# Kernel optimization log

Measured on AMD Instinct MI355X. Metric: run time of the kernel, lower is better.

The kernel has to match this reference:

```python
import jax, jax.numpy as jnp
import numpy as np

QUERY_DIM = 192
KEY_DIM = 64
DIM_OUT = 128
C = QUERY_DIM + KEY_DIM  # 256
N = 10000
E = 320000
M = 5000


def setup_inputs() -> dict:
    key = jax.random.key(0)
    ks = jax.random.split(key, 16)
    s = 1.0 / np.sqrt(C)
    inp = {
        "query": jax.random.normal(ks[0], (N, QUERY_DIM), jnp.float32),
        "key_idx": jax.random.randint(ks[1], (N,), 0, KEY_DIM),
        "edge_index": jax.random.randint(ks[2], (2, E), 0, N),
        "mask_idx": jnp.sort(jax.random.randint(ks[3], (M,), 0, N)),
        "Wq": jax.random.normal(ks[4], (C, C), jnp.float32) * s,
        "bq": jnp.zeros((C,), jnp.float32),
        "Wk": jax.random.normal(ks[5], (C, C), jnp.float32) * s,
        "bk": jnp.zeros((C,), jnp.float32),
        "Wv": jax.random.normal(ks[6], (C, C), jnp.float32) * s,
        "bv": jnp.zeros((C,), jnp.float32),
        "Ws": jax.random.normal(ks[7], (C, C), jnp.float32) * s,
        "bs": jnp.zeros((C,), jnp.float32),
        "Wo": jax.random.normal(ks[8], (KEY_DIM, DIM_OUT), jnp.float32) * (1.0 / np.sqrt(KEY_DIM)),
        "bo": jnp.zeros((DIM_OUT,), jnp.float32),
    }
    return inp


def reference(query, key_idx, edge_index, mask_idx, Wq, bq, Wk, bk, Wv, bv, Ws, bs, Wo, bo):
    # node features: [N, C] = concat(query, one_hot(key))
    x = jnp.concatenate([query, jax.nn.one_hot(key_idx, KEY_DIM, dtype=query.dtype)], axis=1)
    src, dst = edge_index[0], edge_index[1]  # messages flow src -> dst
    # node-level projections (dense GEMMs), then edge gather
    q_n = x @ Wq + bq
    k_n = x @ Wk + bk
    v_n = x @ Wv + bv
    q = q_n[dst]  # [E, C]
    k = k_n[src]
    v = v_n[src]
    score = jnp.sum(q * k, axis=-1) / jnp.sqrt(jnp.asarray(C, x.dtype))  # [E]
    # per-destination softmax over incoming edges
    m = jax.ops.segment_max(score, dst, num_segments=N)  # [N]
    m = jnp.where(jnp.isfinite(m), m, 0.0)
    e = jnp.exp(score - m[dst])
    denom = jax.ops.segment_sum(e, dst, num_segments=N)
    alpha = e / (denom[dst] + 1e-16)
    # scatter-aggregate weighted values + root/skip connection
    agg = jax.ops.segment_sum(alpha[:, None] * v, dst, num_segments=N)  # [N, C]
    out = agg + (x @ Ws + bs)
    h = jax.nn.relu(out[mask_idx])  # [M, C]
    h = h[:, QUERY_DIM:]  # [M, KEY_DIM]
    return h @ Wo + bo  # [M, DIM_OUT]
```

## Files before the change

### kernel.cpp

```cpp
#include <hip/hip_runtime.h>

#define QDIM 192
#define KDIM 64
#define CDIM 256
#define NCOLS 640
#define DOUT 128
#define CAP 128
#define NEG_INF __int_as_float(0xFF800000)

typedef _Float16 hf2 __attribute__((ext_vector_type(2)));
typedef _Float16 half4 __attribute__((ext_vector_type(4)));
typedef _Float16 half8 __attribute__((ext_vector_type(8)));
typedef float floatx4 __attribute__((ext_vector_type(4)));

#if defined(__has_builtin)
#if __has_builtin(__builtin_amdgcn_fdot2)
#define HAVE_FDOT2 1
#endif
#endif

__device__ __forceinline__ hf2 bc_h2(unsigned u) { return __builtin_bit_cast(hf2, u); }

__device__ __forceinline__ float dot2acc(hf2 a, hf2 b, float c) {
#ifdef HAVE_FDOT2
    return __builtin_amdgcn_fdot2(a, b, c, false);
#else
    return c + (float)a[0] * (float)b[0] + (float)a[1] * (float)b[1];
#endif
}

__device__ __forceinline__ void wmap(int j, const float* Wq, const float* Wk,
                                     const float* Wv, const float* Ws,
                                     const float** W, int* wcol) {
    if (j < 256)      { *W = Wq; *wcol = j; }
    else if (j < 512) { *W = Wk; *wcol = j - 256; }
    else if (j < 576) { *W = Wv; *wcol = QDIM + (j - 512); }
    else              { *W = Ws; *wcol = QDIM + (j - 576); }
}

__global__ __launch_bounds__(256) void prep_kernel(
        const float* __restrict__ query,
        const float* Wq, const float* Wk, const float* Wv, const float* Ws,
        _Float16* __restrict__ Qh, _Float16* __restrict__ BhT,
        int* __restrict__ deg, int qchunks, int N) {
    int t = blockIdx.x * blockDim.x + threadIdx.x;
    if (t < qchunks) {
        float4 v = ((const float4*)query)[t];
        half4 h = { (_Float16)v.x, (_Float16)v.y, (_Float16)v.z, (_Float16)v.w };
        ((half4*)Qh)[t] = h;
        return;
    }
    t -= qchunks;
    if (t < NCOLS * QDIM) {
        int n = t / QDIM, k = t % QDIM;
        const float* W; int wc;
        wmap(n, Wq, Wk, Wv, Ws, &W, &wc);
        BhT[t] = (_Float16)W[k * CDIM + wc];
        return;
    }
    t -= NCOLS * QDIM;
    if (t < N) deg[t] = 0;
}

__global__ __launch_bounds__(256) void gemm_scatter(
        const _Float16* __restrict__ Qh, const _Float16* __restrict__ BhT,
        const int* __restrict__ key_idx,
        const float* Wq, const float* bq, const float* Wk, const float* bk,
        const float* Wv, const float* bv, const float* Ws, const float* bs,
        const int* __restrict__ esrc, const int* __restrict__ edst,
        int* __restrict__ deg, int* __restrict__ adj, int E,
        _Float16* __restrict__ Qbuf, _Float16* __restrict__ Kbuf,
        _Float16* __restrict__ Vbuf, float* __restrict__ Sbuf, int N) {
    int tid = threadIdx.x;
    int bm = blockIdx.x * 64;

    {
        int total = gridDim.x * gridDim.y * 256;
        int gid = (blockIdx.y * gridDim.x + blockIdx.x) * 256 + tid;
        for (int e = gid; e < E; e += total) {
            int d = edst[e];
            int slot = atomicAdd(&deg[d], 1);
            if (slot < CAP) adj[d * CAP + slot] = esrc[e];
        }
    }

    int w = tid >> 6, l = tid & 63;
    int lrow = l & 15, quad = l >> 4;

    int gr_a = bm + w * 16 + lrow;
    half8 af[6];
    {
        const _Float16* ap = Qh + (size_t)gr_a * QDIM + quad * 8;
        bool ok = (gr_a < N);
        #pragma unroll
        for (int ks = 0; ks < 6; ks++) {
            half8 z = { (_Float16)0.f, (_Float16)0.f, (_Float16)0.f, (_Float16)0.f,
                        (_Float16)0.f, (_Float16)0.f, (_Float16)0.f, (_Float16)0.f };
            af[ks] = ok ? *(const half8*)(ap + ks * 32) : z;
        }
    }

    int ki[4];
    #pragma unroll
    for (int reg = 0; reg < 4; reg++) {
        int gr = bm + w * 16 + quad * 4 + reg;
        ki[reg] = (gr < N) ? key_idx[gr] : 0;
    }

    #pragma unroll
    for (int t = 0; t < 2; t++) {
        int bn = blockIdx.y * 128 + t * 64;
        const float* Wb; const float* bvec; int wc0;
        if (bn < 256)      { Wb = Wq; bvec = bq; wc0 = bn; }
        else if (bn < 512) { Wb = Wk; bvec = bk; wc0 = bn - 256; }
        else if (bn < 576) { Wb = Wv; bvec = bv; wc0 = QDIM + (bn - 512); }
        else               { Wb = Ws; bvec = bs; wc0 = QDIM + (bn - 576); }

        floatx4 acc[4] = {{0.f,0.f,0.f,0.f},{0.f,0.f,0.f,0.f},{0.f,0.f,0.f,0.f},{0.f,0.f,0.f,0.f}};
        const _Float16* bp = BhT + (size_t)(bn + lrow) * QDIM + quad * 8;
        #pragma unroll
        for (int ks = 0; ks < 6; ks++) {
            #pragma unroll
            for (int nt = 0; nt < 4; nt++) {
                half8 bf = *(const half8*)(bp + (size_t)nt * 16 * QDIM + ks * 32);
                acc[nt] = __builtin_amdgcn_mfma_f32_16x16x32_f16(af[ks], bf, acc[nt], 0, 0, 0);
            }
        }

        #pragma unroll
        for (int nt = 0; nt < 4; nt++) {
            int gc = bn + nt * 16 + lrow;
            int wc = wc0 + nt * 16 + lrow;
            float bias = bvec[wc];
            #pragma unroll
            for (int reg = 0; reg < 4; reg++) {
                int gr = bm + w * 16 + quad * 4 + reg;
                if (gr < N) {
                    float v = acc[nt][reg] + Wb[(size_t)(QDIM + ki[reg]) * CDIM + wc] + bias;
                    if (gc < 256)      Qbuf[(size_t)gr * 256 + gc] = (_Float16)v;
                    else if (gc < 512) Kbuf[(size_t)gr * 256 + (gc - 256)] = (_Float16)v;
                    else if (gc < 576) Vbuf[(size_t)gr * KDIM + (gc - 512)] = (_Float16)v;
                    else               Sbuf[(size_t)gr * KDIM + (gc - 576)] = v;
                }
            }
        }
    }
}

__global__ __launch_bounds__(256) void attend_out(
        const _Float16* __restrict__ Qbuf, const _Float16* __restrict__ Kbuf,
        const _Float16* __restrict__ Vbuf, const float* __restrict__ Sbuf,
        const int* __restrict__ deg, const int* __restrict__ adj,
        const int* __restrict__ mask, const float* __restrict__ Wo,
        const float* __restrict__ bo, float* __restrict__ out, int M) {
    int w = threadIdx.x >> 6, lane = threadIdx.x & 63;
    int r = blockIdx.x * 4 + w;
    if (r >= M) return;
    int node = mask[r];
    if (r > 0 && mask[r - 1] == node) return;
    int l = lane & 15, g = lane >> 4;

    const uint4* qp = (const uint4*)(Qbuf + (size_t)node * 256 + l * 16);
    uint4 qa = qp[0], qb = qp[1];
    hf2 qh[8] = { bc_h2(qa.x), bc_h2(qa.y), bc_h2(qa.z), bc_h2(qa.w),
                  bc_h2(qb.x), bc_h2(qb.y), bc_h2(qb.z), bc_h2(qb.w) };

    int dn = min(deg[node], CAP);
    const int* arow = adj + (size_t)node * CAP;

    float m = NEG_INF, dsum = 0.f;
    float a0 = 0.f, a1 = 0.f, a2 = 0.f, a3 = 0.f;
    for (int i = g; i < dn; i += 4) {
        int s = arow[i];
        const uint4* kp = (const uint4*)(Kbuf + (size_t)s * 256 + l * 16);
        uint4 ka = kp[0], kb = kp[1];
        float d = 0.f;
        d = dot2acc(bc_h2(ka.x), qh[0], d);
        d = dot2acc(bc_h2(ka.y), qh[1], d);
        d = dot2acc(bc_h2(ka.z), qh[2], d);
        d = dot2acc(bc_h2(ka.w), qh[3], d);
        d = dot2acc(bc_h2(kb.x), qh[4], d);
        d = dot2acc(bc_h2(kb.y), qh[5], d);
        d = dot2acc(bc_h2(kb.z), qh[6], d);
        d = dot2acc(bc_h2(kb.w), qh[7], d);
        d += __shfl_xor(d, 1, 64);
        d += __shfl_xor(d, 2, 64);
        d += __shfl_xor(d, 4, 64);
        d += __shfl_xor(d, 8, 64);
        float sc = d * 0.0625f;
        float m_new = fmaxf(m, sc);
        float scale = __expf(m - m_new);
        float p = __expf(sc - m_new);
        dsum = dsum * scale + p;
        uint2 vv = *(const uint2*)(Vbuf + (size_t)s * KDIM + l * 4);
        hf2 v01 = bc_h2(vv.x), v23 = bc_h2(vv.y);
        a0 = a0 * scale + p * (float)v01[0];
        a1 = a1 * scale + p * (float)v01[1];
        a2 = a2 * scale + p * (float)v23[0];
        a3 = a3 * scale + p * (float)v23[1];
        m = m_new;
    }

    float Mx = fmaxf(m, __shfl_xor(m, 16, 64));
    Mx = fmaxf(Mx, __shfl_xor(Mx, 32, 64));
    float wgt = (m == NEG_INF) ? 0.f : __expf(m - Mx);
    float ds = dsum * wgt;
    ds += __shfl_xor(ds, 16, 64);
    ds += __shfl_xor(ds, 32, 64);
    a0 *= wgt; a1 *= wgt; a2 *= wgt; a3 *= wgt;
    a0 += __shfl_xor(a0, 16, 64); a0 += __shfl_xor(a0, 32, 64);
    a1 += __shfl_xor(a1, 16, 64); a1 += __shfl_xor(a1, 32, 64);
    a2 += __shfl_xor(a2, 16, 64); a2 += __shfl_xor(a2, 32, 64);
    a3 += __shfl_xor(a3, 16, 64); a3 += __shfl_xor(a3, 32, 64);
    float inv = 1.f / (ds + 1e-16f);

    float4 s4 = *((const float4*)(Sbuf + (size_t)node * KDIM + l * 4));
    float h0 = fmaxf(a0 * inv + s4.x, 0.f);
    float h1 = fmaxf(a1 * inv + s4.y, 0.f);
    float h2 = fmaxf(a2 * inv + s4.z, 0.f);
    float h3 = fmaxf(a3 * inv + s4.w, 0.f);

    float o0 = bo[lane], o1 = bo[lane + 64];
    #pragma unroll
    for (int c = 0; c < KDIM; c++) {
        float hc = (c & 3) == 0 ? h0 : (c & 3) == 1 ? h1 : (c & 3) == 2 ? h2 : h3;
        float hv = __shfl(hc, c >> 2, 64);
        o0 += hv * Wo[c * DOUT + lane];
        o1 += hv * Wo[c * DOUT + 64 + lane];
    }
    int rr = r;
    do {
        out[(size_t)rr * DOUT + lane] = o0;
        out[(size_t)rr * DOUT + 64 + lane] = o1;
        rr++;
    } while (rr < M && mask[rr] == node);
}

extern "C" void kernel_launch(void* const* d_in, const int* in_sizes, int n_in,
                              void* d_out, int out_size, void* d_ws, size_t ws_size,
                              hipStream_t stream) {
    const float* query    = (const float*)d_in[0];
    const int* key_idx    = (const int*)d_in[1];
    const int* edge_index = (const int*)d_in[2];
    const int* mask_idx   = (const int*)d_in[3];
    const float* Wq = (const float*)d_in[4];
    const float* bq = (const float*)d_in[5];
    const float* Wk = (const float*)d_in[6];
    const float* bk = (const float*)d_in[7];
    const float* Wv = (const float*)d_in[8];
    const float* bv = (const float*)d_in[9];
    const float* Ws = (const float*)d_in[10];
    const float* bs = (const float*)d_in[11];
    const float* Wo = (const float*)d_in[12];
    const float* bo = (const float*)d_in[13];

    int N = in_sizes[0] / QDIM;
    int E = in_sizes[2] / 2;
    int M = in_sizes[3];
    const int* esrc = edge_index;
    const int* edst = edge_index + E;

    char* wsb = (char*)d_ws;
    size_t off = 0;
    auto alloc = [&](size_t nbytes) { char* p = wsb + off; off += (nbytes + 15) & ~15ull; return p; };
    _Float16* Qh   = (_Float16*)alloc((size_t)N * QDIM * 2);
    _Float16* BhT  = (_Float16*)alloc((size_t)NCOLS * QDIM * 2);
    _Float16* Qbuf = (_Float16*)alloc((size_t)N * 256 * 2);
    _Float16* Kbuf = (_Float16*)alloc((size_t)N * 256 * 2);
    _Float16* Vbuf = (_Float16*)alloc((size_t)N * KDIM * 2);
    float* Sbuf    = (float*)alloc((size_t)N * KDIM * 4);
    int*   deg     = (int*)alloc((size_t)N * 4);
    int*   adj     = (int*)alloc((size_t)N * CAP * 4);

    int qchunks = N * QDIM / 4;
    int prep_elems = qchunks + NCOLS * QDIM + N;
    prep_kernel<<<(prep_elems + 255) / 256, 256, 0, stream>>>(
        query, Wq, Wk, Wv, Ws, Qh, BhT, deg, qchunks, N);

    dim3 ggrid((N + 63) / 64, 5);
    gemm_scatter<<<ggrid, 256, 0, stream>>>(Qh, BhT, key_idx, Wq, bq, Wk, bk, Wv, bv,
                                            Ws, bs, esrc, edst, deg, adj, E,
                                            Qbuf, Kbuf, Vbuf, Sbuf, N);

    attend_out<<<(M + 3) / 4, 256, 0, stream>>>(Qbuf, Kbuf, Vbuf, Sbuf, deg, adj,
                                                mask_idx, Wo, bo, (float*)d_out, M);
}
```

Baseline: 157.8 us.

## Split edge scatter into own kernel, skip edges to unmasked nodes, shrink adjacency

The edge-bucketing atomics move out of the GEMM kernel into a separate scatter kernel. The degree array is initialised to a large negative sentinel and reset to zero only for masked destination nodes, so edges whose destination is never read skip the atomic and the adjacency write. Adjacency indices are stored as 16-bit values, halving that traffic, and the GEMM grid now uses one 64-column tile per block for more parallelism. This adds a kernel launch and relies on node ids fitting in 16 bits (N=10000 does).

```diff
diff --git a/kernel.cpp b/kernel.cpp
--- a/kernel.cpp
+++ b/kernel.cpp
@@ -59,30 +59,29 @@
         return;
     }
     t -= NCOLS * QDIM;
-    if (t < N) deg[t] = 0;
-}
-
-__global__ __launch_bounds__(256) void gemm_scatter(
+    if (t < N) deg[t] = (int)0x80000000;
+}
+
+__global__ __launch_bounds__(256) void gemm_nodes(
         const _Float16* __restrict__ Qh, const _Float16* __restrict__ BhT,
         const int* __restrict__ key_idx,
         const float* Wq, const float* bq, const float* Wk, const float* bk,
         const float* Wv, const float* bv, const float* Ws, const float* bs,
-        const int* __restrict__ esrc, const int* __restrict__ edst,
-        int* __restrict__ deg, int* __restrict__ adj, int E,
+        const int* __restrict__ mask, int M, int* __restrict__ deg,
         _Float16* __restrict__ Qbuf, _Float16* __restrict__ Kbuf,
         _Float16* __restrict__ Vbuf, float* __restrict__ Sbuf, int N) {
     int tid = threadIdx.x;
     int bm = blockIdx.x * 64;
-
-    {
-        int total = gridDim.x * gridDim.y * 256;
-        int gid = (blockIdx.y * gridDim.x + blockIdx.x) * 256 + tid;
-        for (int e = gid; e < E; e += total) {
-            int d = edst[e];
-            int slot = atomicAdd(&deg[d], 1);
-            if (slot < CAP) adj[d * CAP + slot] = esrc[e];
-        }
-    }
+    int bn = blockIdx.y * 64;
+
+    int gid = (blockIdx.y * gridDim.x + blockIdx.x) * 256 + tid;
+    if (gid < M) deg[mask[gid]] = 0;
+
+    const float* Wb; const float* bvec; int wc0;
+    if (bn < 256)      { Wb = Wq; bvec = bq; wc0 = bn; }
+    else if (bn < 512) { Wb = Wk; bvec = bk; wc0 = bn - 256; }
+    else if (bn < 576) { Wb = Wv; bvec = bv; wc0 = QDIM + (bn - 512); }
+    else               { Wb = Ws; bvec = bs; wc0 = QDIM + (bn - 576); }
 
     int w = tid >> 6, l = tid & 63;
     int lrow = l & 15, quad = l >> 4;
@@ -100,49 +99,51 @@
         }
     }
 
+    floatx4 acc[4] = {{0.f,0.f,0.f,0.f},{0.f,0.f,0.f,0.f},{0.f,0.f,0.f,0.f},{0.f,0.f,0.f,0.f}};
+    const _Float16* bp = BhT + (size_t)(bn + lrow) * QDIM + quad * 8;
+    #pragma unroll
+    for (int ks = 0; ks < 6; ks++) {
+        #pragma unroll
+        for (int nt = 0; nt < 4; nt++) {
+            half8 bf = *(const half8*)(bp + (size_t)nt * 16 * QDIM + ks * 32);
+            acc[nt] = __builtin_amdgcn_mfma_f32_16x16x32_f16(af[ks], bf, acc[nt], 0, 0, 0);
+        }
+    }
+
     int ki[4];
     #pragma unroll
     for (int reg = 0; reg < 4; reg++) {
         int gr = bm + w * 16 + quad * 4 + reg;
         ki[reg] = (gr < N) ? key_idx[gr] : 0;
     }
-
-    #pragma unroll
-    for (int t = 0; t < 2; t++) {
-        int bn = blockIdx.y * 128 + t * 64;
-        const float* Wb; const float* bvec; int wc0;
-        if (bn < 256)      { Wb = Wq; bvec = bq; wc0 = bn; }
-        else if (bn < 512) { Wb = Wk; bvec = bk; wc0 = bn - 256; }
-        else if (bn < 576) { Wb = Wv; bvec = bv; wc0 = QDIM + (bn - 512); }
-        else               { Wb = Ws; bvec = bs; wc0 = QDIM + (bn - 576); }
-
-        floatx4 acc[4] = {{0.f,0.f,0.f,0.f},{0.f,0.f,0.f,0.f},{0.f,0.f,0.f,0.f},{0.f,0.f,0.f,0.f}};
-        const _Float16* bp = BhT + (size_t)(bn + lrow) * QDIM + quad * 8;
+    #pragma unroll
+    for (int nt = 0; nt < 4; nt++) {
+        int gc = bn + nt * 16 + lrow;
+        int wc = wc0 + nt * 16 + lrow;
+        float bias = bvec[wc];
         #pragma unroll
-        for (int ks = 0; ks < 6; ks++) {
-            #pragma unroll
-            for (int nt = 0; nt < 4; nt++) {
-                half8 bf = *(const half8*)(bp + (size_t)nt * 16 * QDIM + ks * 32);
-                acc[nt] = __builtin_amdgcn_mfma_f32_16x16x32_f16(af[ks], bf, acc[nt], 0, 0, 0);
+        for (int reg = 0; reg < 4; reg++) {
+            int gr = bm + w * 16 + quad * 4 + reg;
+            if (gr < N) {
+                float v = acc[nt][reg] + Wb[(size_t)(QDIM + ki[reg]) * CDIM + wc] + bias;
+                if (gc < 256)      Qbuf[(size_t)gr * 256 + gc] = (_Float16)v;
+                else if (gc < 512) Kbuf[(size_t)gr * 256 + (gc - 256)] = (_Float16)v;
+                else if (gc < 576) Vbuf[(size_t)gr * KDIM + (gc - 512)] = (_Float16)v;
+                else               Sbuf[(size_t)gr * KDIM + (gc - 576)] = v;
             }
         }
-
-        #pragma unroll
-        for (int nt = 0; nt < 4; nt++) {
-            int gc = bn + nt * 16 + lrow;
-            int wc = wc0 + nt * 16 + lrow;
-            float bias = bvec[wc];
-            #pragma unroll
-            for (int reg = 0; reg < 4; reg++) {
-                int gr = bm + w * 16 + quad * 4 + reg;
-                if (gr < N) {
-                    float v = acc[nt][reg] + Wb[(size_t)(QDIM + ki[reg]) * CDIM + wc] + bias;
-                    if (gc < 256)      Qbuf[(size_t)gr * 256 + gc] = (_Float16)v;
-                    else if (gc < 512) Kbuf[(size_t)gr * 256 + (gc - 256)] = (_Float16)v;
-                    else if (gc < 576) Vbuf[(size_t)gr * KDIM + (gc - 512)] = (_Float16)v;
-                    else               Sbuf[(size_t)gr * KDIM + (gc - 576)] = v;
-                }
-            }
+    }
+}
+
+__global__ __launch_bounds__(256) void scatter_kernel(
+        const int* __restrict__ src, const int* __restrict__ dst,
+        int* __restrict__ deg, unsigned short* __restrict__ adj, int E) {
+    int e = blockIdx.x * blockDim.x + threadIdx.x;
+    if (e < E) {
+        int d = dst[e];
+        if (deg[d] > -1000000) {
+            int slot = atomicAdd(&deg[d], 1);
+            if ((unsigned)slot < CAP) adj[(size_t)d * CAP + slot] = (unsigned short)src[e];
         }
     }
 }
@@ -150,7 +151,7 @@
 __global__ __launch_bounds__(256) void attend_out(
         const _Float16* __restrict__ Qbuf, const _Float16* __restrict__ Kbuf,
         const _Float16* __restrict__ Vbuf, const float* __restrict__ Sbuf,
-        const int* __restrict__ deg, const int* __restrict__ adj,
+        const int* __restrict__ deg, const unsigned short* __restrict__ adj,
         const int* __restrict__ mask, const float* __restrict__ Wo,
         const float* __restrict__ bo, float* __restrict__ out, int M) {
     int w = threadIdx.x >> 6, lane = threadIdx.x & 63;
@@ -166,7 +167,7 @@
                   bc_h2(qb.x), bc_h2(qb.y), bc_h2(qb.z), bc_h2(qb.w) };
 
     int dn = min(deg[node], CAP);
-    const int* arow = adj + (size_t)node * CAP;
+    const unsigned short* arow = adj + (size_t)node * CAP;
 
     float m = NEG_INF, dsum = 0.f;
     float a0 = 0.f, a1 = 0.f, a2 = 0.f, a3 = 0.f;
@@ -270,17 +271,19 @@
     _Float16* Vbuf = (_Float16*)alloc((size_t)N * KDIM * 2);
     float* Sbuf    = (float*)alloc((size_t)N * KDIM * 4);
     int*   deg     = (int*)alloc((size_t)N * 4);
-    int*   adj     = (int*)alloc((size_t)N * CAP * 4);
+    unsigned short* adj = (unsigned short*)alloc((size_t)N * CAP * 2);
 
     int qchunks = N * QDIM / 4;
     int prep_elems = qchunks + NCOLS * QDIM + N;
     prep_kernel<<<(prep_elems + 255) / 256, 256, 0, stream>>>(
         query, Wq, Wk, Wv, Ws, Qh, BhT, deg, qchunks, N);
 
-    dim3 ggrid((N + 63) / 64, 5);
-    gemm_scatter<<<ggrid, 256, 0, stream>>>(Qh, BhT, key_idx, Wq, bq, Wk, bk, Wv, bv,
-                                            Ws, bs, esrc, edst, deg, adj, E,
-                                            Qbuf, Kbuf, Vbuf, Sbuf, N);
+    dim3 ggrid((N + 63) / 64, 10);
+    gemm_nodes<<<ggrid, 256, 0, stream>>>(Qh, BhT, key_idx, Wq, bq, Wk, bk, Wv, bv,
+                                          Ws, bs, mask_idx, M, deg,
+                                          Qbuf, Kbuf, Vbuf, Sbuf, N);
+
+    scatter_kernel<<<(E + 255) / 256, 256, 0, stream>>>(esrc, edst, deg, adj, E);
 
     attend_out<<<(M + 3) / 4, 256, 0, stream>>>(Qbuf, Kbuf, Vbuf, Sbuf, deg, adj,
                                                 mask_idx, Wo, bo, (float*)d_out, M);
```

After: 154.6 us. -2.0%, faster.
